# Kernel optimization log

Measured on AMD Instinct MI355X. Metric: run time of the kernel, lower is better.

## Reference

```python
import jax, jax.numpy as jnp
import numpy as np

B, N, F, H, F_ = 2048, 8192, 512, 8, 64

def setup_inputs() -> dict:
    key = jax.random.key(0)
    k1, k2, k3, k4 = jax.random.split(key, 4)
    X = jax.random.normal(k1, (B, F), dtype=jnp.float32)
    G = jax.random.normal(k2, (N, F), dtype=jnp.float32)
    W = jax.random.normal(k3, (H, F, F_), dtype=jnp.float32) * 0.05   # per-head kernels
    att = jax.random.normal(k4, (H, 2 * F_), dtype=jnp.float32) * 0.05  # per-head att kernels (2F_,1) flattened
    return {"X": X, "G": G, "W": W, "att": att}

def reference(X, G, W, att):
    f_ = W.shape[-1]
    # Per-head linear transforms
    WhX = jnp.einsum('bf,hfe->hbe', X, W)   # [H,B,F_]
    WhG = jnp.einsum('nf,hfe->hne', G, W)   # [H,N,F_]
    # concat([WhX_i, WhG_j]) @ a  ==  WhX_i @ a1 + WhG_j @ a2  -> avoids tiled [B*N,2F_]
    a1, a2 = att[:, :f_], att[:, f_:]
    e1 = jnp.einsum('hbe,he->hb', WhX, a1)  # [H,B]
    e2 = jnp.einsum('hne,he->hn', WhG, a2)  # [H,N]
    scores = e1[:, :, None] + e2[:, None, :]            # [H,B,N] pairwise logits
    attn = jax.nn.softmax(scores, axis=-1)              # softmax over graph nodes
    out = jnp.einsum('hbn,hne->hbe', attn, WhG)         # weighted aggregate [H,B,F_]
    out = jax.nn.relu(out)                              # concat-mode applies activation per head
    # concat heads -> [B, H*F_]
    return jnp.transpose(out, (1, 0, 2)).reshape(out.shape[1], -1)
```

## Files before the change

kernel.cpp:

```cpp
#include <hip/hip_runtime.h>


#define HF   8
#define FDIM 512
#define FE   64
#define NG   8192
#define BX   2048
#define MB   256
#define ROWS 32

__global__ __launch_bounds__(256) void k_w2(const float* __restrict__ W,
                                            const float* __restrict__ att,
                                            float* __restrict__ w2) {
    int gid = blockIdx.x * 256 + threadIdx.x;
    int o = gid >> 1, half = gid & 1;
    int h = o >> 9, f = o & 511;
    const float* a2 = att + h * (2 * FE) + FE + half * 32;
    const float* wp = W + ((size_t)(h * FDIM + f)) * FE + half * 32;
    float s = 0.f;
#pragma unroll
    for (int e = 0; e < 32; e += 4) {
        float4 w4 = *reinterpret_cast<const float4*>(wp + e);
        s += w4.x * a2[e] + w4.y * a2[e + 1] + w4.z * a2[e + 2] + w4.w * a2[e + 3];
    }
    s += __shfl_xor(s, 1, 64);
    if (half == 0) w2[o] = s;
}

__global__ __launch_bounds__(256) void k_main(const float* __restrict__ G,
                                              const float* __restrict__ w2g,
                                              float* __restrict__ part,
                                              float* __restrict__ s_part) {
    __shared__ float lds[HF * FDIM];
    __shared__ float s_lds[4 * HF];
    int bid = blockIdx.x, tid = threadIdx.x;
    int wave = tid >> 6, lane = tid & 63;

    float4 w2a[HF], w2b[HF];
#pragma unroll
    for (int h = 0; h < HF; ++h) {
        const float* wp = w2g + h * FDIM + lane * 8;
        w2a[h] = *reinterpret_cast<const float4*>(wp);
        w2b[h] = *reinterpret_cast<const float4*>(wp + 4);
    }
    float4 accA[HF], accB[HF];
#pragma unroll
    for (int h = 0; h < HF; ++h) {
        accA[h] = make_float4(0.f, 0.f, 0.f, 0.f);
        accB[h] = make_float4(0.f, 0.f, 0.f, 0.f);
    }
    float s_acc[HF] = {};

    int n0 = bid * ROWS + wave * (ROWS / 4);
    for (int r = 0; r < ROWS / 4; ++r) {
        const float* gp = G + (size_t)(n0 + r) * FDIM + lane * 8;
        float4 g0 = *reinterpret_cast<const float4*>(gp);
        float4 g1 = *reinterpret_cast<const float4*>(gp + 4);
        float e[HF];
#pragma unroll
        for (int h = 0; h < HF; ++h)
            e[h] = g0.x * w2a[h].x + g0.y * w2a[h].y + g0.z * w2a[h].z + g0.w * w2a[h].w
                 + g1.x * w2b[h].x + g1.y * w2b[h].y + g1.z * w2b[h].z + g1.w * w2b[h].w;
#pragma unroll
        for (int off = 32; off > 0; off >>= 1) {
#pragma unroll
            for (int h = 0; h < HF; ++h) e[h] += __shfl_xor(e[h], off, 64);
        }
#pragma unroll
        for (int h = 0; h < HF; ++h) {
            float w = __expf(e[h]);
            s_acc[h] += w;
            accA[h].x = fmaf(w, g0.x, accA[h].x);
            accA[h].y = fmaf(w, g0.y, accA[h].y);
            accA[h].z = fmaf(w, g0.z, accA[h].z);
            accA[h].w = fmaf(w, g0.w, accA[h].w);
            accB[h].x = fmaf(w, g1.x, accB[h].x);
            accB[h].y = fmaf(w, g1.y, accB[h].y);
            accB[h].z = fmaf(w, g1.z, accB[h].z);
            accB[h].w = fmaf(w, g1.w, accB[h].w);
        }
    }

    for (int w = 0; w < 4; ++w) {
        if (wave == w) {
#pragma unroll
            for (int h = 0; h < HF; ++h) {
                float* dst = lds + h * FDIM + lane * 8;
                if (w == 0) {
                    *reinterpret_cast<float4*>(dst)     = accA[h];
                    *reinterpret_cast<float4*>(dst + 4) = accB[h];
                } else {
                    float4 t0 = *reinterpret_cast<float4*>(dst);
                    float4 t1 = *reinterpret_cast<float4*>(dst + 4);
                    t0.x += accA[h].x; t0.y += accA[h].y; t0.z += accA[h].z; t0.w += accA[h].w;
                    t1.x += accB[h].x; t1.y += accB[h].y; t1.z += accB[h].z; t1.w += accB[h].w;
                    *reinterpret_cast<float4*>(dst)     = t0;
                    *reinterpret_cast<float4*>(dst + 4) = t1;
                }
            }
            if (lane == 0) {
#pragma unroll
                for (int h = 0; h < HF; ++h) s_lds[w * HF + h] = s_acc[h];
            }
        }
        __syncthreads();
    }

    float* dst = part + (size_t)bid * (HF * FDIM);
    for (int i = tid; i < HF * FDIM; i += 256) dst[i] = lds[i];
    if (tid < HF)
        s_part[bid * HF + tid] =
            (s_lds[tid] + s_lds[HF + tid]) + (s_lds[2 * HF + tid] + s_lds[3 * HF + tid]);
}

__global__ __launch_bounds__(256) void k_gredvr(const float* __restrict__ part,
                                                const float* __restrict__ W,
                                                float* __restrict__ vr_part) {
    int bid = blockIdx.x;
    int h = bid >> 3, f0 = (bid & 7) * 64;
    int tid = threadIdx.x, lane = tid & 63, wv = tid >> 6;

    float v = 0.f;
    int elem = h * FDIM + f0 + lane;
#pragma unroll 8
    for (int j = 0; j < MB / 4; ++j)
        v += part[(size_t)(wv * (MB / 4) + j) * (HF * FDIM) + elem];
    __shared__ float gs[4][64];
    gs[wv][lane] = v;
    __syncthreads();
    __shared__ float g_slice[64];
    if (tid < 64)
        g_slice[tid] = (gs[0][tid] + gs[1][tid]) + (gs[2][tid] + gs[3][tid]);
    __syncthreads();

    float acc = 0.f;
    const float* wp = W + (size_t)h * FDIM * FE + (size_t)(f0 + wv * 16) * FE + lane;
#pragma unroll
    for (int f = 0; f < 16; ++f)
        acc = fmaf(g_slice[wv * 16 + f], wp[(size_t)f * FE], acc);
    __shared__ float vp[4][64];
    vp[wv][lane] = acc;
    __syncthreads();
    if (tid < 64)
        vr_part[bid * 64 + tid] = (vp[0][tid] + vp[1][tid]) + (vp[2][tid] + vp[3][tid]);
}

__global__ __launch_bounds__(256) void k_final(const float* __restrict__ vr_part,
                                               const float* __restrict__ s_part,
                                               float* __restrict__ out) {
    __shared__ float vr[HF * FE];
    __shared__ float s_tmp[64];
    __shared__ float s_h[HF];
    int bid = blockIdx.x, tid = threadIdx.x;

    if (tid < 64) {
        int h = tid & 7, c = tid >> 3;
        float sv = 0.f;
#pragma unroll
        for (int j = 0; j < 32; ++j) sv += s_part[(c * 32 + j) * HF + h];
        s_tmp[tid] = sv;
    }
    __syncthreads();
    if (tid < HF) {
        float t = 0.f;
#pragma unroll
        for (int c = 0; c < 8; ++c) t += s_tmp[c * 8 + tid];
        s_h[tid] = t;
    }
    __syncthreads();

#pragma unroll
    for (int r = 0; r < 2; ++r) {
        int o = tid + r * 256;
        int h = o >> 6, e = o & 63;
        float v = 0.f;
#pragma unroll
        for (int k = 0; k < 8; ++k) v += vr_part[(h * 8 + k) * 64 + e];
        vr[o] = fmaxf(v / s_h[h], 0.f);
    }
    __syncthreads();

    const float4* v4 = reinterpret_cast<const float4*>(vr);
    float4* o4 = reinterpret_cast<float4*>(out);
    for (int i = tid; i < 8 * 128; i += 256) {
        int row = i >> 7, c = i & 127;
        o4[(size_t)(bid * 8 + row) * 128 + c] = v4[c];
    }
}

extern "C" void kernel_launch(void* const* d_in, const int* in_sizes, int n_in,
                              void* d_out, int out_size, void* d_ws, size_t ws_size,
                              hipStream_t stream) {
    const float* G   = (const float*)d_in[1];
    const float* W   = (const float*)d_in[2];
    const float* att = (const float*)d_in[3];
    float* out = (float*)d_out;

    float* ws      = (float*)d_ws;
    float* w2      = ws;
    float* s_part  = ws + 4096;
    float* vr_part = ws + 6144;
    float* part    = ws + 10240;

    k_w2    <<<32,  256, 0, stream>>>(W, att, w2);
    k_main  <<<MB,  256, 0, stream>>>(G, w2, part, s_part);
    k_gredvr<<<64,  256, 0, stream>>>(part, W, vr_part);
    k_final <<<256, 256, 0, stream>>>(vr_part, s_part, out);
}
```

Before: 38.87 us.

## Fuse main, reduction and final kernels with atomics and a grid barrier

Collapses the four-kernel pipeline into two launches. An init kernel zeroes the accumulators and computes w2. The fused kernel atomically accumulates the per-block partial sums into a global buffer, then waits at a spin-wait grid barrier on a counter. After the barrier each block computes a 16-column slice of the W projection for one head and writes its share of the broadcast output rows. This removes two launches and the partial-buffer round trip, but relies on all 256 blocks being co-resident and makes the float sums order-nondeterministic.

```diff
diff --git a/kernel.cpp b/kernel.cpp
--- a/kernel.cpp
+++ b/kernel.cpp
@@ -6,35 +6,55 @@
 #define FE   64
 #define NG   8192
 #define BX   2048
-#define MB   256
-#define ROWS 32
+#define K2B  256
+#define ROWS (NG / K2B)
 
-__global__ __launch_bounds__(256) void k_w2(const float* __restrict__ W,
-                                            const float* __restrict__ att,
-                                            float* __restrict__ w2) {
-    int gid = blockIdx.x * 256 + threadIdx.x;
-    int o = gid >> 1, half = gid & 1;
-    int h = o >> 9, f = o & 511;
-    const float* a2 = att + h * (2 * FE) + FE + half * 32;
-    const float* wp = W + ((size_t)(h * FDIM + f)) * FE + half * 32;
+#define WS_W2 16
+#define WS_G  4224
+#define WS_S  8384
+
+__global__ __launch_bounds__(256) void k_init(const float* __restrict__ W,
+                                              const float* __restrict__ att,
+                                              float* __restrict__ ws) {
+    int bid = blockIdx.x, tid = threadIdx.x;
+    int idx = bid * 256 + tid;
+    if (idx < 4096) ws[WS_G + idx] = 0.f;
+    if (idx >= 4096 && idx < 4104) ws[WS_S + (idx - 4096)] = 0.f;
+    if (idx == 4104) *reinterpret_cast<unsigned int*>(ws) = 0u;
+
+    int o = bid * 64 + (tid >> 2);
+    int sub = tid & 3;
+    int h = o >> 9;
+    const float* wp = W + (size_t)o * FE + sub * 16;
+    const float* a2 = att + h * (2 * FE) + FE + sub * 16;
     float s = 0.f;
 #pragma unroll
-    for (int e = 0; e < 32; e += 4) {
+    for (int e = 0; e < 16; e += 4) {
         float4 w4 = *reinterpret_cast<const float4*>(wp + e);
         s += w4.x * a2[e] + w4.y * a2[e + 1] + w4.z * a2[e + 2] + w4.w * a2[e + 3];
     }
     s += __shfl_xor(s, 1, 64);
-    if (half == 0) w2[o] = s;
+    s += __shfl_xor(s, 2, 64);
+    if (sub == 0) ws[WS_W2 + o] = s;
 }
 
-__global__ __launch_bounds__(256) void k_main(const float* __restrict__ G,
-                                              const float* __restrict__ w2g,
-                                              float* __restrict__ part,
-                                              float* __restrict__ s_part) {
+__global__ __launch_bounds__(256, 1) void k_fused(const float* __restrict__ G,
+                                                  const float* __restrict__ W,
+                                                  float* __restrict__ ws,
+                                                  float* __restrict__ out) {
     __shared__ float lds[HF * FDIM];
     __shared__ float s_lds[4 * HF];
+    __shared__ float gh[FDIM];
+    __shared__ float vp[16][17];
+    __shared__ float vrs[16];
+    __shared__ float s_h_lds;
+
     int bid = blockIdx.x, tid = threadIdx.x;
     int wave = tid >> 6, lane = tid & 63;
+    const float* w2g = ws + WS_W2;
+    float* g = ws + WS_G;
+    float* sdenom = ws + WS_S;
+    unsigned int* counter = reinterpret_cast<unsigned int*>(ws);
 
     float4 w2a[HF], w2b[HF];
 #pragma unroll
@@ -106,86 +126,58 @@
         __syncthreads();
     }
 
-    float* dst = part + (size_t)bid * (HF * FDIM);
-    for (int i = tid; i < HF * FDIM; i += 256) dst[i] = lds[i];
+    for (int i = tid; i < HF * FDIM; i += 256) atomicAdd(&g[i], lds[i]);
     if (tid < HF)
-        s_part[bid * HF + tid] =
-            (s_lds[tid] + s_lds[HF + tid]) + (s_lds[2 * HF + tid] + s_lds[3 * HF + tid]);
-}
+        atomicAdd(&sdenom[tid],
+                  (s_lds[tid] + s_lds[HF + tid]) + (s_lds[2 * HF + tid] + s_lds[3 * HF + tid]));
 
-__global__ __launch_bounds__(256) void k_gredvr(const float* __restrict__ part,
-                                                const float* __restrict__ W,
-                                                float* __restrict__ vr_part) {
-    int bid = blockIdx.x;
-    int h = bid >> 3, f0 = (bid & 7) * 64;
-    int tid = threadIdx.x, lane = tid & 63, wv = tid >> 6;
+    __threadfence();
+    __syncthreads();
+    if (tid == 0) {
+        atomicAdd(counter, 1u);
+        int iters = 0;
+        while (__hip_atomic_load(counter, __ATOMIC_ACQUIRE, __HIP_MEMORY_SCOPE_AGENT) < K2B) {
+            __builtin_amdgcn_s_sleep(2);
+            if (++iters > 2000000) break;
+        }
+    }
+    __syncthreads();
+    __threadfence();
 
-    float v = 0.f;
-    int elem = h * FDIM + f0 + lane;
-#pragma unroll 8
-    for (int j = 0; j < MB / 4; ++j)
-        v += part[(size_t)(wv * (MB / 4) + j) * (HF * FDIM) + elem];
-    __shared__ float gs[4][64];
-    gs[wv][lane] = v;
-    __syncthreads();
-    __shared__ float g_slice[64];
-    if (tid < 64)
-        g_slice[tid] = (gs[0][tid] + gs[1][tid]) + (gs[2][tid] + gs[3][tid]);
+    int slice = bid & 31, rowchunk = bid >> 5;
+    int h = slice >> 2, e0 = (slice & 3) * 16;
+
+    for (int i = tid; i < FDIM; i += 256)
+        gh[i] = __hip_atomic_load(&g[h * FDIM + i], __ATOMIC_RELAXED, __HIP_MEMORY_SCOPE_AGENT);
+    if (tid == 0)
+        s_h_lds = __hip_atomic_load(&sdenom[h], __ATOMIC_RELAXED, __HIP_MEMORY_SCOPE_AGENT);
     __syncthreads();
 
-    float acc = 0.f;
-    const float* wp = W + (size_t)h * FDIM * FE + (size_t)(f0 + wv * 16) * FE + lane;
-#pragma unroll
-    for (int f = 0; f < 16; ++f)
-        acc = fmaf(g_slice[wv * 16 + f], wp[(size_t)f * FE], acc);
-    __shared__ float vp[4][64];
-    vp[wv][lane] = acc;
-    __syncthreads();
-    if (tid < 64)
-        vr_part[bid * 64 + tid] = (vp[0][tid] + vp[1][tid]) + (vp[2][tid] + vp[3][tid]);
-}
-
-__global__ __launch_bounds__(256) void k_final(const float* __restrict__ vr_part,
-                                               const float* __restrict__ s_part,
-                                               float* __restrict__ out) {
-    __shared__ float vr[HF * FE];
-    __shared__ float s_tmp[64];
-    __shared__ float s_h[HF];
-    int bid = blockIdx.x, tid = threadIdx.x;
-
-    if (tid < 64) {
-        int h = tid & 7, c = tid >> 3;
-        float sv = 0.f;
-#pragma unroll
-        for (int j = 0; j < 32; ++j) sv += s_part[(c * 32 + j) * HF + h];
-        s_tmp[tid] = sv;
+    int j = tid & 15, fg = tid >> 4;
+    {
+        const float* wp = W + ((size_t)(h * FDIM + fg * 32)) * FE + e0 + j;
+        float acc = 0.f;
+#pragma unroll 8
+        for (int k = 0; k < 32; ++k)
+            acc = fmaf(gh[fg * 32 + k], wp[(size_t)k * FE], acc);
+        vp[fg][j] = acc;
     }
     __syncthreads();
-    if (tid < HF) {
-        float t = 0.f;
+    if (tid < 16) {
+        float v = 0.f;
 #pragma unroll
-        for (int c = 0; c < 8; ++c) t += s_tmp[c * 8 + tid];
-        s_h[tid] = t;
+        for (int k = 0; k < 16; ++k) v += vp[k][tid];
+        vrs[tid] = fmaxf(v / s_h_lds, 0.f);
     }
     __syncthreads();
 
-#pragma unroll
-    for (int r = 0; r < 2; ++r) {
-        int o = tid + r * 256;
-        int h = o >> 6, e = o & 63;
-        float v = 0.f;
-#pragma unroll
-        for (int k = 0; k < 8; ++k) v += vr_part[(h * 8 + k) * 64 + e];
-        vr[o] = fmaxf(v / s_h[h], 0.f);
-    }
-    __syncthreads();
-
-    const float4* v4 = reinterpret_cast<const float4*>(vr);
-    float4* o4 = reinterpret_cast<float4*>(out);
-    for (int i = tid; i < 8 * 128; i += 256) {
-        int row = i >> 7, c = i & 127;
-        o4[(size_t)(bid * 8 + row) * 128 + c] = v4[c];
-    }
+    int r = rowchunk * 256 + tid;
+    float4* dst = reinterpret_cast<float4*>(out + (size_t)r * FDIM + h * FE + e0);
+    float4 o0 = make_float4(vrs[0],  vrs[1],  vrs[2],  vrs[3]);
+    float4 o1 = make_float4(vrs[4],  vrs[5],  vrs[6],  vrs[7]);
+    float4 o2 = make_float4(vrs[8],  vrs[9],  vrs[10], vrs[11]);
+    float4 o3 = make_float4(vrs[12], vrs[13], vrs[14], vrs[15]);
+    dst[0] = o0; dst[1] = o1; dst[2] = o2; dst[3] = o3;
 }
 
 extern "C" void kernel_launch(void* const* d_in, const int* in_sizes, int n_in,
@@ -195,15 +187,8 @@
     const float* W   = (const float*)d_in[2];
     const float* att = (const float*)d_in[3];
     float* out = (float*)d_out;
+    float* ws  = (float*)d_ws;
 
-    float* ws      = (float*)d_ws;
-    float* w2      = ws;
-    float* s_part  = ws + 4096;
-    float* vr_part = ws + 6144;
-    float* part    = ws + 10240;
-
-    k_w2    <<<32,  256, 0, stream>>>(W, att, w2);
-    k_main  <<<MB,  256, 0, stream>>>(G, w2, part, s_part);
-    k_gredvr<<<64,  256, 0, stream>>>(part, W, vr_part);
-    k_final <<<256, 256, 0, stream>>>(vr_part, s_part, out);
+    k_init <<<64,  256, 0, stream>>>(W, att, ws);
+    k_fused<<<K2B, 256, 0, stream>>>(G, W, ws, out);
 }
```

Result: slower. 80.07 us (+106.0%).
